# Kernel tuning notes

Measured on AMD Instinct MI355X. Metric: run time of the kernel, lower is better.

The kernel has to match this reference:

```python
import itertools
import jax, jax.numpy as jnp
import numpy as np

N_QUBITS = 8
N_LAYERS = 2
BATCH = 8192
INPUT_DIM = 3072
NUM_CLASSES = 10

_In = np.eye(2, dtype=np.complex64)
_Xn = np.array([[0, 1], [1, 0]], dtype=np.complex64)
_Yn = np.array([[0, -1j], [1j, 0]], dtype=np.complex64)
_Zn = np.array([[1, 0], [0, -1]], dtype=np.complex64)
_P = {"I": _In, "X": _Xn, "Y": _Yn, "Z": _Zn}
_XX = jnp.asarray(np.kron(_Xn, _Xn))
_YY = jnp.asarray(np.kron(_Yn, _Yn))
_ZZ = jnp.asarray(np.kron(_Zn, _Zn))
_I4 = jnp.eye(4, dtype=jnp.complex64)
# 2-qubit Pauli words in PennyLane ArbitraryUnitary order: IX, IY, IZ, XI, ..., ZZ
_WORDS = jnp.asarray(np.stack([np.kron(_P[a], _P[b]) for a, b in itertools.product("IXYZ", repeat=2)][1:]))


def apply_gate(state, U, wires):
    """Apply a 2^k x 2^k gate U to the given wires of a (2,)*n statevector."""
    n = state.ndim
    k = len(wires)
    U = U.reshape((2,) * (2 * k)).astype(state.dtype)
    state = jnp.tensordot(U, state, axes=(list(range(k, 2 * k)), list(wires)))
    rest = [a for a in range(n) if a not in wires]
    perm = [0] * n
    for i, a in enumerate(wires):
        perm[a] = i
    for j, a in enumerate(rest):
        perm[a] = k + j
    return jnp.transpose(state, perm)


def u3_mat(t, p, d):
    ct, st = jnp.cos(t / 2).astype(jnp.complex64), jnp.sin(t / 2).astype(jnp.complex64)
    r0 = jnp.stack([ct, -jnp.exp(1j * d) * st])
    r1 = jnp.stack([jnp.exp(1j * p) * st, jnp.exp(1j * (p + d)) * ct])
    return jnp.stack([r0, r1])


def ry_mat(t):
    c, s = jnp.cos(t / 2), jnp.sin(t / 2)
    return jnp.stack([jnp.stack([c, -s]), jnp.stack([s, c])]).astype(jnp.complex64)


def ising_mat(phi, pauli2):
    # exp(-i phi/2 P) for two-qubit Pauli word P (P^2 = I)
    return jnp.cos(phi / 2) * _I4 - 1j * jnp.sin(phi / 2) * pauli2


def circuit(conv_w, pool_w, last_w, feats):
    state = jnp.zeros((2,) * N_QUBITS, jnp.complex64).at[(0,) * N_QUBITS].set(1.0)
    # AngleEmbedding with RY rotations
    for w in range(N_QUBITS):
        state = apply_gate(state, ry_mat(feats[w]), (w,))
    wires = list(range(N_QUBITS))
    for layer in range(N_LAYERS):
        cw = conv_w[layer]
        nw = len(wires)
        for p in (0, 1):
            for idx in range(nw - 1):
                if idx % 2 == p:
                    a, b = wires[idx], wires[idx + 1]
                    state = apply_gate(state, u3_mat(cw[idx, 0], cw[idx, 1], cw[idx, 2]), (a,))
                    state = apply_gate(state, u3_mat(cw[idx + 1, 3], cw[idx + 1, 4], cw[idx + 1, 5]), (b,))
                    state = apply_gate(state, ising_mat(cw[idx, 6], _ZZ), (a, b))
                    state = apply_gate(state, ising_mat(cw[idx, 7], _YY), (a, b))
                    state = apply_gate(state, ising_mat(cw[idx, 8], _XX), (a, b))
                    state = apply_gate(state, u3_mat(cw[idx, 9], cw[idx, 10], cw[idx, 11]), (a,))
                    state = apply_gate(state, u3_mat(cw[idx + 1, 12], cw[idx + 1, 13], cw[idx + 1, 14]), (b,))
        # Pooling: mid-circuit measure + conditional U3 == (deferred measurement)
        pw = pool_w[layer]
        for idx in range(1, nw, 2):
            u = u3_mat(pw[idx // 2, 0], pw[idx // 2, 1], pw[idx // 2, 2])
            cu = jnp.zeros((4, 4), jnp.complex64).at[0, 0].set(1.0).at[1, 1].set(1.0).at[2:, 2:].set(u)
            state = apply_gate(state, cu, (wires[idx], wires[idx - 1]))
        wires = wires[::2]
    # ArbitraryUnitary on remaining 2 wires: product of 15 PauliRot gates
    for k in range(15):
        mat = jnp.cos(last_w[k] / 2) * _I4 - 1j * jnp.sin(last_w[k] / 2) * _WORDS[k]
        state = apply_gate(state, mat, tuple(wires))
    probs = state.real ** 2 + state.imag ** 2
    z = jnp.sum(probs, axis=tuple(range(1, N_QUBITS)))  # (2,)
    return z[0] - z[1]


def setup_inputs() -> dict:
    key = jax.random.key(0)
    ks = jax.random.split(key, 8)
    return {
        "x": jax.random.normal(ks[0], (BATCH, INPUT_DIM), jnp.float32),
        "fc_w": jax.random.normal(ks[1], (N_QUBITS, INPUT_DIM), jnp.float32) * 0.02,
        "fc_b": jnp.zeros((N_QUBITS,), jnp.float32),
        "conv_params": jax.random.normal(ks[2], (N_LAYERS, N_QUBITS, 15), jnp.float32),
        "pool_params": jax.random.normal(ks[3], (N_LAYERS, N_QUBITS // 2, 3), jnp.float32),
        "last_params": jax.random.normal(ks[4], (15,), jnp.float32),
        "out_w": jax.random.normal(ks[5], (NUM_CLASSES, 1), jnp.float32),
        "out_b": jnp.zeros((NUM_CLASSES,), jnp.float32),
    }


def reference(x, fc_w, fc_b, conv_params, pool_params, last_params, out_w, out_b):
    feats = jnp.tanh(x.reshape(x.shape[0], -1) @ fc_w.T + fc_b)  # (B, n_qubits)
    qvals = jax.vmap(lambda f: circuit(conv_params, pool_params, last_params, f))(feats)
    logits = qvals[:, None].astype(x.dtype) @ out_w.T + out_b  # (B, num_classes)
    return logits
```

## Files before the change

kernel.cpp:

```cpp
#include <hip/hip_runtime.h>
#include <math.h>

__constant__ int G_ORD[17] = {0,1,2,3,4,5,6, 10,11,12,13, 7,8,9, 14,15, 16};
__constant__ int G_WA[17]  = {0,2,4,6,1,3,5, 1,3,5,7, 0,4,2, 2,6, 0};
__constant__ int G_WB[17]  = {1,3,5,7,2,4,6, 0,2,4,6, 2,6,4, 0,4, 4};
__constant__ int CDESC[10][3] = {{0,0,1},{0,2,3},{0,4,5},{0,6,7},{0,1,2},{0,3,4},{0,5,6},
                                 {1,0,1},{1,2,3},{1,1,2}};
__constant__ int PDESC[6][2] = {{0,0},{0,1},{0,2},{0,3},{1,0},{1,1}};
__constant__ float2 PMAT[4][4] = {
  {{1.f,0.f},{0.f,0.f},{0.f,0.f},{1.f,0.f}},
  {{0.f,0.f},{1.f,0.f},{1.f,0.f},{0.f,0.f}},
  {{0.f,0.f},{0.f,-1.f},{0.f,1.f},{0.f,0.f}},
  {{1.f,0.f},{0.f,0.f},{0.f,0.f},{-1.f,0.f}}};

__device__ __forceinline__ float2 cmul(float2 a, float2 b){
  return make_float2(a.x*b.x - a.y*b.y, a.x*b.y + a.y*b.x);
}
__device__ __forceinline__ float2 cadd(float2 a, float2 b){
  return make_float2(a.x+b.x, a.y+b.y);
}

__device__ void u3m(float t, float p, float d, float2* u){
  float ct = cosf(0.5f*t), st = sinf(0.5f*t);
  u[0] = make_float2(ct, 0.f);
  u[1] = make_float2(-cosf(d)*st, -sinf(d)*st);
  u[2] = make_float2(cosf(p)*st,  sinf(p)*st);
  u[3] = make_float2(cosf(p+d)*ct, sinf(p+d)*ct);
}

__device__ void kron2(const float2* A, const float2* B, float2* M){
  #pragma unroll
  for (int ia=0; ia<2; ia++)
    #pragma unroll
    for (int ib=0; ib<2; ib++)
      #pragma unroll
      for (int ja=0; ja<2; ja++)
        #pragma unroll
        for (int jb=0; jb<2; jb++)
          M[(ia*2+ib)*4 + (ja*2+jb)] = cmul(A[ia*2+ja], B[ib*2+jb]);
}

__device__ void mul44(const float2* A, const float2* B, float2* C){
  #pragma unroll
  for (int r=0;r<4;r++)
    #pragma unroll
    for (int c=0;c<4;c++){
      float2 s = make_float2(0.f,0.f);
      #pragma unroll
      for (int k=0;k<4;k++) s = cadd(s, cmul(A[r*4+k], B[k*4+c]));
      C[r*4+c] = s;
    }
}

__device__ void rotword(float phi, int qa, int qb, float2* R){
  float ch = cosf(0.5f*phi), sh = sinf(0.5f*phi);
  float2 W[16];
  kron2(PMAT[qa], PMAT[qb], W);
  #pragma unroll
  for (int i=0;i<16;i++) R[i] = make_float2(sh*W[i].y, -sh*W[i].x);
  #pragma unroll
  for (int d=0;d<4;d++) R[d*4+d].x += ch;
}

__global__ __launch_bounds__(64) void build_gates_kernel(
    const float* __restrict__ conv, const float* __restrict__ pool,
    const float* __restrict__ last, float* __restrict__ gates){
  int t = threadIdx.x;
  float2 M[16], T[16], R[16];
  if (t < 10){
    int layer = CDESC[t][0], ra = CDESC[t][1], rb = CDESC[t][2];
    const float* cw = conv + layer*120;
    int bA = ra*15, bB = rb*15;
    float2 A1[4], B1[4], A2[4], B2[4], K[16];
    u3m(cw[bA+0], cw[bA+1], cw[bA+2], A1);
    u3m(cw[bB+3], cw[bB+4], cw[bB+5], B1);
    kron2(A1, B1, M);
    rotword(cw[bA+6], 3, 3, R); mul44(R, M, T);
    rotword(cw[bA+7], 2, 2, R); mul44(R, T, M);
    rotword(cw[bA+8], 1, 1, R); mul44(R, M, T);
    u3m(cw[bA+9],  cw[bA+10], cw[bA+11], A2);
    u3m(cw[bB+12], cw[bB+13], cw[bB+14], B2);
    kron2(A2, B2, K); mul44(K, T, M);
  } else if (t < 16){
    int layer = PDESC[t-10][0], h = PDESC[t-10][1];
    const float* pw = pool + layer*12 + h*3;
    float2 u[4];
    u3m(pw[0], pw[1], pw[2], u);
    #pragma unroll
    for (int i=0;i<16;i++) M[i] = make_float2(0.f,0.f);
    M[0]  = make_float2(1.f,0.f);
    M[5]  = make_float2(1.f,0.f);
    M[10] = u[0]; M[11] = u[1]; M[14] = u[2]; M[15] = u[3];
  } else if (t == 16){
    #pragma unroll
    for (int i=0;i<16;i++) M[i] = make_float2((i%5==0)?1.f:0.f, 0.f);
    for (int k=0;k<15;k++){
      int w = k+1;
      rotword(last[k], w>>2, w&3, R);
      mul44(R, M, T);
      #pragma unroll
      for (int i=0;i<16;i++) M[i] = T[i];
    }
  }
  if (t < 17){
    float2* dst = (float2*)(gates + t*32);
    #pragma unroll
    for (int i=0;i<16;i++) dst[i] = M[i];
  }
}

__global__ __launch_bounds__(64) void build_u_kernel(
    const float* __restrict__ gates, float2* __restrict__ U){
  __shared__ float2 st[256];
  int lane = threadIdx.x, col = blockIdx.x;
  #pragma unroll
  for (int k=lane; k<256; k+=64) st[k] = make_float2(k==col ? 1.f : 0.f, 0.f);
  __syncthreads();
  for (int g=0; g<17; g++){
    int slot = G_ORD[g];
    const float2* gm = (const float2*)(gates + slot*32);
    float2 m[16];
    #pragma unroll
    for (int i=0;i<16;i++) m[i] = gm[i];
    int pa = 7 - G_WA[g], pb = 7 - G_WB[g];
    int plo = pa < pb ? pa : pb, phi_ = pa < pb ? pb : pa;
    int mm = lane;
    int t1   = ((mm >> plo) << (plo+1)) | (mm & ((1<<plo)-1));
    int base = ((t1 >> phi_) << (phi_+1)) | (t1 & ((1<<phi_)-1));
    int ba = 1<<pa, bb = 1<<pb;
    int i0 = base, i1 = base|bb, i2 = base|ba, i3 = base|ba|bb;
    float2 s0 = st[i0], s1 = st[i1], s2 = st[i2], s3 = st[i3];
    float2 n0 = cadd(cadd(cmul(m[0], s0), cmul(m[1], s1)), cadd(cmul(m[2], s2), cmul(m[3], s3)));
    float2 n1 = cadd(cadd(cmul(m[4], s0), cmul(m[5], s1)), cadd(cmul(m[6], s2), cmul(m[7], s3)));
    float2 n2 = cadd(cadd(cmul(m[8], s0), cmul(m[9], s1)), cadd(cmul(m[10],s2), cmul(m[11],s3)));
    float2 n3 = cadd(cadd(cmul(m[12],s0), cmul(m[13],s1)), cadd(cmul(m[14],s2), cmul(m[15],s3)));
    st[i0] = n0; st[i1] = n1; st[i2] = n2; st[i3] = n3;
    __syncthreads();
  }
  #pragma unroll
  for (int k=lane; k<256; k+=64) U[k*256 + col] = st[k];
}

__global__ __launch_bounds__(256) void build_a_kernel(
    const float2* __restrict__ U, float* __restrict__ A){
  int j = threadIdx.x, i0 = blockIdx.x*2;
  float a0=0.f, a1=0.f;
  #pragma unroll 8
  for (int k=0; k<256; k++){
    float2 uj = U[k*256 + j];
    float2 u0 = U[k*256 + i0+0];
    float2 u1 = U[k*256 + i0+1];
    float sgn = (k < 128) ? 1.f : -1.f;
    a0 += sgn*(u0.x*uj.x + u0.y*uj.y);
    a1 += sgn*(u1.x*uj.x + u1.y*uj.y);
  }
  A[(i0+0)*256 + j] = a0;
  A[(i0+1)*256 + j] = a1;
}

__global__ __launch_bounds__(256) void feats_kernel(
    const float* __restrict__ x, const float* __restrict__ fcw,
    const float* __restrict__ fcb, float* __restrict__ feats){
  __shared__ float red[128*68];
  int t = threadIdx.x, lane = t & 63, wv = t >> 6;
  int r0 = blockIdx.x * 16;
  int rw = r0 + wv*4;
  const float4* x4 = (const float4*)x;
  const float4* w4 = (const float4*)fcw;
  float acc[4][8];
  #pragma unroll
  for (int r=0;r<4;r++)
    #pragma unroll
    for (int o=0;o<8;o++) acc[r][o] = 0.f;
  for (int p=0; p<12; p++){
    float4 wf[8];
    #pragma unroll
    for (int o=0;o<8;o++) wf[o] = w4[o*768 + p*64 + lane];
    #pragma unroll
    for (int r=0;r<4;r++){
      float4 xv = x4[(size_t)(rw+r)*768 + p*64 + lane];
      #pragma unroll
      for (int o=0;o<8;o++){
        acc[r][o] += xv.x*wf[o].x + xv.y*wf[o].y + xv.z*wf[o].z + xv.w*wf[o].w;
      }
    }
  }
  #pragma unroll
  for (int r=0;r<4;r++)
    #pragma unroll
    for (int o=0;o<8;o++)
      red[((wv*4+r)*8 + o)*68 + lane] = acc[r][o];
  __syncthreads();
  if (t < 128){
    const float4* rp = (const float4*)(red + t*68);
    float4 s4 = make_float4(0.f,0.f,0.f,0.f);
    #pragma unroll
    for (int i=0;i<16;i++){
      float4 v = rp[i];
      s4.x += v.x; s4.y += v.y; s4.z += v.z; s4.w += v.w;
    }
    float s = s4.x + s4.y + s4.z + s4.w + fcb[t & 7];
    feats[(r0 + (t>>3))*8 + (t&7)] = tanhf(s);
  }
}

__global__ __launch_bounds__(256) void qform_kernel(
    const float* __restrict__ Ag, const float* __restrict__ feats,
    const float* __restrict__ outw, const float* __restrict__ outb,
    float* __restrict__ out){
  __shared__ float As[32*256];
  __shared__ float ps[16*256];
  int t = threadIdx.x;
  int r0 = blockIdx.x * 16;
  {
    int row = t >> 4, i1 = t & 15;
    const float* f = feats + (r0 + row)*8;
    float c[8], s[8];
    #pragma unroll
    for (int w=0; w<8; w++){
      float a = 0.5f*f[w];
      __sincosf(a, &s[w], &c[w]);
    }
    float Hv = (i1&8 ? s[0]:c[0]) * (i1&4 ? s[1]:c[1])
             * (i1&2 ? s[2]:c[2]) * (i1&1 ? s[3]:c[3]);
    float l2[2], l4[4], l8[8], L[16];
    l2[0]=c[4]; l2[1]=s[4];
    #pragma unroll
    for (int a=0;a<2;a++){ l4[a*2]=l2[a]*c[5]; l4[a*2+1]=l2[a]*s[5]; }
    #pragma unroll
    for (int a=0;a<4;a++){ l8[a*2]=l4[a]*c[6]; l8[a*2+1]=l4[a]*s[6]; }
    #pragma unroll
    for (int a=0;a<8;a++){ L[a*2]=l8[a]*c[7]; L[a*2+1]=l8[a]*s[7]; }
    float* dst = ps + row*256 + i1*16;
    #pragma unroll
    for (int j=0;j<16;j++) dst[j] = Hv*L[j];
  }
  int wv = t >> 6, jb = t & 63;
  const float4* As4 = (const float4*)As;
  const float4* ps4 = (const float4*)ps;
  float4 acc4[4];
  #pragma unroll
  for (int r=0;r<4;r++) acc4[r] = make_float4(0.f,0.f,0.f,0.f);
  for (int chunk=0; chunk<8; chunk++){
    __syncthreads();
    #pragma unroll
    for (int pass=0; pass<8; pass++){
      int kk = pass*4 + wv;
      *(float4*)(As + kk*256 + jb*4) =
        *(const float4*)(Ag + (chunk*32 + kk)*256 + jb*4);
    }
    __syncthreads();
    #pragma unroll
    for (int kk4=0; kk4<8; kk4++){
      float4 av0 = As4[(kk4*4+0)*64 + jb];
      float4 av1 = As4[(kk4*4+1)*64 + jb];
      float4 av2 = As4[(kk4*4+2)*64 + jb];
      float4 av3 = As4[(kk4*4+3)*64 + jb];
      #pragma unroll
      for (int r=0; r<4; r++){
        float4 pv = ps4[(wv*4+r)*64 + chunk*8 + kk4];
        acc4[r].x += pv.x*av0.x + pv.y*av1.x + pv.z*av2.x + pv.w*av3.x;
        acc4[r].y += pv.x*av0.y + pv.y*av1.y + pv.z*av2.y + pv.w*av3.y;
        acc4[r].z += pv.x*av0.z + pv.y*av1.z + pv.z*av2.z + pv.w*av3.z;
        acc4[r].w += pv.x*av0.w + pv.y*av1.w + pv.z*av2.w + pv.w*av3.w;
      }
    }
  }
  float p[4];
  #pragma unroll
  for (int r=0; r<4; r++){
    float4 psv = ps4[(wv*4+r)*64 + jb];
    float pr = acc4[r].x*psv.x + acc4[r].y*psv.y + acc4[r].z*psv.z + acc4[r].w*psv.w;
    #pragma unroll
    for (int m=1; m<64; m<<=1) pr += __shfl_xor(pr, m, 64);
    p[r] = pr;
  }
  if (jb < 40){
    int ridx = jb / 10, c = jb - ridx*10;
    float q = (ridx==0) ? p[0] : (ridx==1) ? p[1] : (ridx==2) ? p[2] : p[3];
    out[(r0 + wv*4 + ridx)*10 + c] = q*outw[c] + outb[c];
  }
}

extern "C" void kernel_launch(void* const* d_in, const int* in_sizes, int n_in,
                              void* d_out, int out_size, void* d_ws, size_t ws_size,
                              hipStream_t stream) {
  const float* x    = (const float*)d_in[0];
  const float* fcw  = (const float*)d_in[1];
  const float* fcb  = (const float*)d_in[2];
  const float* conv = (const float*)d_in[3];
  const float* pool = (const float*)d_in[4];
  const float* last = (const float*)d_in[5];
  const float* outw = (const float*)d_in[6];
  const float* outb = (const float*)d_in[7];
  float* out = (float*)d_out;

  float* ws = (float*)d_ws;
  float*  gates = ws;
  float2* U     = (float2*)(ws + 1024);
  float*  Am    = ws + 1024 + 131072;
  float*  feats = Am + 65536;

  build_gates_kernel<<<1, 64, 0, stream>>>(conv, pool, last, gates);
  build_u_kernel<<<256, 64, 0, stream>>>(gates, U);
  build_a_kernel<<<128, 256, 0, stream>>>(U, Am);
  feats_kernel<<<512, 256, 0, stream>>>(x, fcw, fcb, feats);
  qform_kernel<<<512, 256, 0, stream>>>(Am, feats, outw, outb, out);
}
```

Measured before the change: 259.0 us.

## Fuse gate building into unitary kernel and feats projection into quadratic-form kernel

Gate-matrix construction now runs inside each build_u block, with results held in shared memory. This removes a single-block launch and a global round-trip, at the cost of every one of the 256 blocks recomputing the gates. The feature projection and tanh are fused into the quadratic-form kernel, which keeps features in LDS and reuses one shared buffer for the reduction, the A tile and the psi tile. The intent is to cut launch overhead and feats global traffic. The trade-off is higher per-block LDS use and a longer kernel that may lower occupancy.

```diff
diff --git a/kernel.cpp b/kernel.cpp
--- a/kernel.cpp
+++ b/kernel.cpp
@@ -62,69 +62,65 @@
   for (int d=0;d<4;d++) R[d*4+d].x += ch;
 }
 
-__global__ __launch_bounds__(64) void build_gates_kernel(
+__global__ __launch_bounds__(64) void build_u_kernel(
     const float* __restrict__ conv, const float* __restrict__ pool,
-    const float* __restrict__ last, float* __restrict__ gates){
-  int t = threadIdx.x;
-  float2 M[16], T[16], R[16];
-  if (t < 10){
-    int layer = CDESC[t][0], ra = CDESC[t][1], rb = CDESC[t][2];
-    const float* cw = conv + layer*120;
-    int bA = ra*15, bB = rb*15;
-    float2 A1[4], B1[4], A2[4], B2[4], K[16];
-    u3m(cw[bA+0], cw[bA+1], cw[bA+2], A1);
-    u3m(cw[bB+3], cw[bB+4], cw[bB+5], B1);
-    kron2(A1, B1, M);
-    rotword(cw[bA+6], 3, 3, R); mul44(R, M, T);
-    rotword(cw[bA+7], 2, 2, R); mul44(R, T, M);
-    rotword(cw[bA+8], 1, 1, R); mul44(R, M, T);
-    u3m(cw[bA+9],  cw[bA+10], cw[bA+11], A2);
-    u3m(cw[bB+12], cw[bB+13], cw[bB+14], B2);
-    kron2(A2, B2, K); mul44(K, T, M);
-  } else if (t < 16){
-    int layer = PDESC[t-10][0], h = PDESC[t-10][1];
-    const float* pw = pool + layer*12 + h*3;
-    float2 u[4];
-    u3m(pw[0], pw[1], pw[2], u);
-    #pragma unroll
-    for (int i=0;i<16;i++) M[i] = make_float2(0.f,0.f);
-    M[0]  = make_float2(1.f,0.f);
-    M[5]  = make_float2(1.f,0.f);
-    M[10] = u[0]; M[11] = u[1]; M[14] = u[2]; M[15] = u[3];
-  } else if (t == 16){
-    #pragma unroll
-    for (int i=0;i<16;i++) M[i] = make_float2((i%5==0)?1.f:0.f, 0.f);
-    for (int k=0;k<15;k++){
-      int w = k+1;
-      rotword(last[k], w>>2, w&3, R);
-      mul44(R, M, T);
-      #pragma unroll
-      for (int i=0;i<16;i++) M[i] = T[i];
-    }
-  }
-  if (t < 17){
-    float2* dst = (float2*)(gates + t*32);
-    #pragma unroll
-    for (int i=0;i<16;i++) dst[i] = M[i];
-  }
-}
-
-__global__ __launch_bounds__(64) void build_u_kernel(
-    const float* __restrict__ gates, float2* __restrict__ U){
+    const float* __restrict__ last, float2* __restrict__ U){
+  __shared__ float2 gl[17][16];
   __shared__ float2 st[256];
-  int lane = threadIdx.x, col = blockIdx.x;
-  #pragma unroll
-  for (int k=lane; k<256; k+=64) st[k] = make_float2(k==col ? 1.f : 0.f, 0.f);
+  int t = threadIdx.x, col = blockIdx.x;
+  {
+    float2 M[16], T[16], R[16];
+    if (t < 10){
+      int layer = CDESC[t][0], ra = CDESC[t][1], rb = CDESC[t][2];
+      const float* cw = conv + layer*120;
+      int bA = ra*15, bB = rb*15;
+      float2 A1[4], B1[4], A2[4], B2[4], K[16];
+      u3m(cw[bA+0], cw[bA+1], cw[bA+2], A1);
+      u3m(cw[bB+3], cw[bB+4], cw[bB+5], B1);
+      kron2(A1, B1, M);
+      rotword(cw[bA+6], 3, 3, R); mul44(R, M, T);
+      rotword(cw[bA+7], 2, 2, R); mul44(R, T, M);
+      rotword(cw[bA+8], 1, 1, R); mul44(R, M, T);
+      u3m(cw[bA+9],  cw[bA+10], cw[bA+11], A2);
+      u3m(cw[bB+12], cw[bB+13], cw[bB+14], B2);
+      kron2(A2, B2, K); mul44(K, T, M);
+    } else if (t < 16){
+      int layer = PDESC[t-10][0], h = PDESC[t-10][1];
+      const float* pw = pool + layer*12 + h*3;
+      float2 u[4];
+      u3m(pw[0], pw[1], pw[2], u);
+      #pragma unroll
+      for (int i=0;i<16;i++) M[i] = make_float2(0.f,0.f);
+      M[0]  = make_float2(1.f,0.f);
+      M[5]  = make_float2(1.f,0.f);
+      M[10] = u[0]; M[11] = u[1]; M[14] = u[2]; M[15] = u[3];
+    } else if (t == 16){
+      #pragma unroll
+      for (int i=0;i<16;i++) M[i] = make_float2((i%5==0)?1.f:0.f, 0.f);
+      for (int k=0;k<15;k++){
+        int w = k+1;
+        rotword(last[k], w>>2, w&3, R);
+        mul44(R, M, T);
+        #pragma unroll
+        for (int i=0;i<16;i++) M[i] = T[i];
+      }
+    }
+    if (t < 17){
+      #pragma unroll
+      for (int i=0;i<16;i++) gl[t][i] = M[i];
+    }
+  }
+  #pragma unroll
+  for (int k=t; k<256; k+=64) st[k] = make_float2(k==col ? 1.f : 0.f, 0.f);
   __syncthreads();
   for (int g=0; g<17; g++){
     int slot = G_ORD[g];
-    const float2* gm = (const float2*)(gates + slot*32);
     float2 m[16];
     #pragma unroll
-    for (int i=0;i<16;i++) m[i] = gm[i];
+    for (int i=0;i<16;i++) m[i] = gl[slot][i];
     int pa = 7 - G_WA[g], pb = 7 - G_WB[g];
     int plo = pa < pb ? pa : pb, phi_ = pa < pb ? pb : pa;
-    int mm = lane;
+    int mm = t;
     int t1   = ((mm >> plo) << (plo+1)) | (mm & ((1<<plo)-1));
     int base = ((t1 >> phi_) << (phi_+1)) | (t1 & ((1<<phi_)-1));
     int ba = 1<<pa, bb = 1<<pb;
@@ -138,7 +134,7 @@
     __syncthreads();
   }
   #pragma unroll
-  for (int k=lane; k<256; k+=64) U[k*256 + col] = st[k];
+  for (int k=t; k<256; k+=64) U[k*256 + col] = st[k];
 }
 
 __global__ __launch_bounds__(256) void build_a_kernel(
@@ -158,38 +154,47 @@
   A[(i0+1)*256 + j] = a1;
 }
 
-__global__ __launch_bounds__(256) void feats_kernel(
+__global__ __launch_bounds__(256) void main_kernel(
     const float* __restrict__ x, const float* __restrict__ fcw,
-    const float* __restrict__ fcb, float* __restrict__ feats){
-  __shared__ float red[128*68];
-  int t = threadIdx.x, lane = t & 63, wv = t >> 6;
+    const float* __restrict__ fcb, const float* __restrict__ Ag,
+    const float* __restrict__ outw, const float* __restrict__ outb,
+    float* __restrict__ out){
+  __shared__ float lds[12288];
+  __shared__ float flds[128];
+  float* red = lds;
+  float* As  = lds;
+  float* ps  = lds + 8192;
+  int t = threadIdx.x, lane = t & 63, wv = t >> 6, jb = lane;
   int r0 = blockIdx.x * 16;
-  int rw = r0 + wv*4;
-  const float4* x4 = (const float4*)x;
-  const float4* w4 = (const float4*)fcw;
-  float acc[4][8];
-  #pragma unroll
-  for (int r=0;r<4;r++)
-    #pragma unroll
-    for (int o=0;o<8;o++) acc[r][o] = 0.f;
-  for (int p=0; p<12; p++){
-    float4 wf[8];
-    #pragma unroll
-    for (int o=0;o<8;o++) wf[o] = w4[o*768 + p*64 + lane];
-    #pragma unroll
-    for (int r=0;r<4;r++){
-      float4 xv = x4[(size_t)(rw+r)*768 + p*64 + lane];
-      #pragma unroll
-      for (int o=0;o<8;o++){
-        acc[r][o] += xv.x*wf[o].x + xv.y*wf[o].y + xv.z*wf[o].z + xv.w*wf[o].w;
+  {
+    int rw = r0 + wv*4;
+    const float4* x4 = (const float4*)x;
+    const float4* w4 = (const float4*)fcw;
+    float acc[4][8];
+    #pragma unroll
+    for (int r=0;r<4;r++)
+      #pragma unroll
+      for (int o=0;o<8;o++) acc[r][o] = 0.f;
+    #pragma unroll 2
+    for (int p=0; p<12; p++){
+      float4 wf[8];
+      #pragma unroll
+      for (int o=0;o<8;o++) wf[o] = w4[o*768 + p*64 + lane];
+      #pragma unroll
+      for (int r=0;r<4;r++){
+        float4 xv = x4[(size_t)(rw+r)*768 + p*64 + lane];
+        #pragma unroll
+        for (int o=0;o<8;o++){
+          acc[r][o] += xv.x*wf[o].x + xv.y*wf[o].y + xv.z*wf[o].z + xv.w*wf[o].w;
+        }
       }
     }
-  }
-  #pragma unroll
-  for (int r=0;r<4;r++)
-    #pragma unroll
-    for (int o=0;o<8;o++)
-      red[((wv*4+r)*8 + o)*68 + lane] = acc[r][o];
+    #pragma unroll
+    for (int r=0;r<4;r++)
+      #pragma unroll
+      for (int o=0;o<8;o++)
+        red[((wv*4+r)*8 + o)*68 + lane] = acc[r][o];
+  }
   __syncthreads();
   if (t < 128){
     const float4* rp = (const float4*)(red + t*68);
@@ -199,22 +204,13 @@
       float4 v = rp[i];
       s4.x += v.x; s4.y += v.y; s4.z += v.z; s4.w += v.w;
     }
-    float s = s4.x + s4.y + s4.z + s4.w + fcb[t & 7];
-    feats[(r0 + (t>>3))*8 + (t&7)] = tanhf(s);
-  }
-}
-
-__global__ __launch_bounds__(256) void qform_kernel(
-    const float* __restrict__ Ag, const float* __restrict__ feats,
-    const float* __restrict__ outw, const float* __restrict__ outb,
-    float* __restrict__ out){
-  __shared__ float As[32*256];
-  __shared__ float ps[16*256];
-  int t = threadIdx.x;
-  int r0 = blockIdx.x * 16;
+    flds[t] = tanhf(s4.x + s4.y + s4.z + s4.w + fcb[t & 7]);
+  }
+  __syncthreads();
+  float psi_local[16];
   {
     int row = t >> 4, i1 = t & 15;
-    const float* f = feats + (r0 + row)*8;
+    const float* f = flds + row*8;
     float c[8], s[8];
     #pragma unroll
     for (int w=0; w<8; w++){
@@ -231,13 +227,21 @@
     for (int a=0;a<4;a++){ l8[a*2]=l4[a]*c[6]; l8[a*2+1]=l4[a]*s[6]; }
     #pragma unroll
     for (int a=0;a<8;a++){ L[a*2]=l8[a]*c[7]; L[a*2+1]=l8[a]*s[7]; }
-    float* dst = ps + row*256 + i1*16;
-    #pragma unroll
-    for (int j=0;j<16;j++) dst[j] = Hv*L[j];
-  }
-  int wv = t >> 6, jb = t & 63;
+    #pragma unroll
+    for (int j=0;j<16;j++) psi_local[j] = Hv*L[j];
+  }
+  __syncthreads();
+  {
+    int row = t >> 4, i1 = t & 15;
+    float4* dst = (float4*)(ps + row*256 + i1*16);
+    #pragma unroll
+    for (int qd=0; qd<4; qd++)
+      dst[qd] = make_float4(psi_local[qd*4+0], psi_local[qd*4+1],
+                            psi_local[qd*4+2], psi_local[qd*4+3]);
+  }
   const float4* As4 = (const float4*)As;
   const float4* ps4 = (const float4*)ps;
+  const float4* Ag4 = (const float4*)Ag;
   float4 acc4[4];
   #pragma unroll
   for (int r=0;r<4;r++) acc4[r] = make_float4(0.f,0.f,0.f,0.f);
@@ -246,19 +250,18 @@
     #pragma unroll
     for (int pass=0; pass<8; pass++){
       int kk = pass*4 + wv;
-      *(float4*)(As + kk*256 + jb*4) =
-        *(const float4*)(Ag + (chunk*32 + kk)*256 + jb*4);
+      *(float4*)(As + kk*256 + jb*4) = Ag4[(chunk*32 + kk)*64 + jb];
     }
     __syncthreads();
     #pragma unroll
-    for (int kk4=0; kk4<8; kk4++){
-      float4 av0 = As4[(kk4*4+0)*64 + jb];
-      float4 av1 = As4[(kk4*4+1)*64 + jb];
-      float4 av2 = As4[(kk4*4+2)*64 + jb];
-      float4 av3 = As4[(kk4*4+3)*64 + jb];
+    for (int kq=0; kq<8; kq++){
+      float4 av0 = As4[(kq*4+0)*64 + jb];
+      float4 av1 = As4[(kq*4+1)*64 + jb];
+      float4 av2 = As4[(kq*4+2)*64 + jb];
+      float4 av3 = As4[(kq*4+3)*64 + jb];
       #pragma unroll
       for (int r=0; r<4; r++){
-        float4 pv = ps4[(wv*4+r)*64 + chunk*8 + kk4];
+        float4 pv = ps4[(wv*4+r)*64 + chunk*8 + kq];
         acc4[r].x += pv.x*av0.x + pv.y*av1.x + pv.z*av2.x + pv.w*av3.x;
         acc4[r].y += pv.x*av0.y + pv.y*av1.y + pv.z*av2.y + pv.w*av3.y;
         acc4[r].z += pv.x*av0.z + pv.y*av1.z + pv.z*av2.z + pv.w*av3.z;
@@ -296,14 +299,10 @@
   float* out = (float*)d_out;
 
   float* ws = (float*)d_ws;
-  float*  gates = ws;
-  float2* U     = (float2*)(ws + 1024);
-  float*  Am    = ws + 1024 + 131072;
-  float*  feats = Am + 65536;
-
-  build_gates_kernel<<<1, 64, 0, stream>>>(conv, pool, last, gates);
-  build_u_kernel<<<256, 64, 0, stream>>>(gates, U);
+  float2* U  = (float2*)ws;
+  float*  Am = ws + 131072;
+
+  build_u_kernel<<<256, 64, 0, stream>>>(conv, pool, last, U);
   build_a_kernel<<<128, 256, 0, stream>>>(U, Am);
-  feats_kernel<<<512, 256, 0, stream>>>(x, fcw, fcb, feats);
-  qform_kernel<<<512, 256, 0, stream>>>(Am, feats, outw, outb, out);
-}
+  main_kernel<<<512, 256, 0, stream>>>(x, fcw, fcb, Am, outw, outb, out);
+}
```

Measured after the change: 244.7 us. 5.5% less time.
